# Kernel optimization log

Hardware: AMD Instinct MI355X
Metric: run time of the kernel (lower is better)

## Reference

```python
import jax, jax.numpy as jnp
import numpy as np

B, S, D = 4, 4096, 256


def setup_inputs() -> dict:
    key = jax.random.key(0)
    ks = jax.random.split(key, 7)
    s = 1.0 / np.sqrt(D)
    return {
        "x": jax.random.normal(ks[0], (B, S, D), dtype=jnp.float32),
        "Wq": jax.random.uniform(ks[1], (D, D), jnp.float32, -s, s),
        "bq": jax.random.uniform(ks[2], (D,), jnp.float32, -s, s),
        "Wk": jax.random.uniform(ks[3], (D, D), jnp.float32, -s, s),
        "bk": jax.random.uniform(ks[4], (D,), jnp.float32, -s, s),
        "Wv": jax.random.uniform(ks[5], (D, D), jnp.float32, -s, s),
        "bv": jax.random.uniform(ks[6], (D,), jnp.float32, -s, s),
    }


def reference(x, Wq, bq, Wk, bk, Wv, bv):
    # nn.Linear: y = x @ W.T + b
    Q = jnp.einsum("bsd,ed->bse", x, Wq) + bq
    K = jnp.einsum("bsd,ed->bse", x, Wk) + bk
    V = jnp.einsum("bsd,ed->bse", x, Wv) + bv
    dk = Q.shape[-1]
    scores = jnp.einsum("bqd,bkd->bqk", Q, K) / jnp.sqrt(jnp.float32(dk))
    # NOTE: original applies softmax over dim=1 (the query axis), not -1.
    attn = jax.nn.softmax(scores, axis=1)
    out = jnp.einsum("bqk,bkd->bqd", attn, V)
    return out
```

## Files before the change

### kernel.cpp

```cpp
#include <hip/hip_runtime.h>

typedef short bf16x8 __attribute__((ext_vector_type(8)));
typedef float f32x4 __attribute__((ext_vector_type(4)));
typedef unsigned short u16;

#define S_LEN 4096
#define D_DIM 256
#define NROW  16384

__device__ __forceinline__ u16 f2bf(float f) {
    union { float f; unsigned u; } v; v.f = f;
    unsigned r = v.u + 0x7FFFu + ((v.u >> 16) & 1u);
    return (u16)(r >> 16);
}

__device__ __forceinline__ size_t fr_qk(int t, int kk) {
    return (size_t)t * 4096 + kk * 512;
}
__device__ __forceinline__ size_t fr_v(int p, int dt, int kk2) {
    return (size_t)p * 16384 + (dt * 2 + kk2) * 512;
}

__device__ __forceinline__ void gll16(const u16* g, u16* l) {
    __builtin_amdgcn_global_load_lds(
        (const __attribute__((address_space(1))) unsigned int*)g,
        (__attribute__((address_space(3))) unsigned int*)l, 16, 0, 0);
}

#define WAITV4 asm volatile("s_waitcnt vmcnt(4)" ::: "memory")
#define WAITV0 asm volatile("s_waitcnt vmcnt(0)" ::: "memory")
#define WAITLGKM0 asm volatile("s_waitcnt lgkmcnt(0)" ::: "memory")
#define MEMFENCE asm volatile("" ::: "memory")

__global__ __launch_bounds__(256) void wconv(
    const float* __restrict__ Wq, const float* __restrict__ Wk,
    const float* __restrict__ Wv, u16* __restrict__ Wf)
{
    int i = blockIdx.x * 256 + threadIdx.x;
    int m = i >> 13;
    int idx = i & 8191;
    int ocol = idx >> 5;
    int d0 = (idx & 31) * 8;
    const float* s = (m == 0 ? Wq : (m == 1 ? Wk : Wv)) + ocol * 256 + d0;
    float4 v0 = *reinterpret_cast<const float4*>(s);
    float4 v1 = *reinterpret_cast<const float4*>(s + 4);
    union { ushort4 h[2]; int4 q; } t;
    t.h[0] = make_ushort4(f2bf(v0.x), f2bf(v0.y), f2bf(v0.z), f2bf(v0.w));
    t.h[1] = make_ushort4(f2bf(v1.x), f2bf(v1.y), f2bf(v1.z), f2bf(v1.w));
    size_t off = (size_t)m * 65536 + fr_qk(ocol >> 4, d0 >> 5)
               + ((d0 >> 3) & 3) * 128 + (ocol & 15) * 8;
    *reinterpret_cast<int4*>(Wf + off) = t.q;
}

__global__ __launch_bounds__(256) void qkv_proj(
    const float* __restrict__ x, const u16* __restrict__ Wf,
    const float* __restrict__ bq, const float* __restrict__ bk,
    const float* __restrict__ bv,
    u16* __restrict__ Qf, u16* __restrict__ Kf, u16* __restrict__ Vf)
{
    __shared__ u16 xs[32][264];
    const int tid = threadIdx.x;
    const int r0 = blockIdx.x * 32;

    #pragma unroll
    for (int i = 0; i < 8; ++i) {
        int c = i * 256 + tid;
        int row = c >> 6, c4 = c & 63;
        float4 v = reinterpret_cast<const float4*>(x + (size_t)(r0 + row) * D_DIM)[c4];
        *reinterpret_cast<ushort4*>(&xs[row][c4 * 4]) =
            make_ushort4(f2bf(v.x), f2bf(v.y), f2bf(v.z), f2bf(v.w));
    }
    __syncthreads();

    const int w = tid >> 6, l = tid & 63, lr = l & 15, lg = l >> 4;
    const int c0 = w * 64;

    bf16x8 a[2][8];
    #pragma unroll
    for (int qs = 0; qs < 2; ++qs)
        #pragma unroll
        for (int kk = 0; kk < 8; ++kk)
            a[qs][kk] = *reinterpret_cast<const bf16x8*>(&xs[qs * 16 + lr][kk * 32 + lg * 8]);

    const float* Bs[3] = {bq, bk, bv};

    #pragma unroll
    for (int m = 0; m < 3; ++m) {
        const u16* Wm = Wf + (size_t)m * 65536;
        f32x4 acc[2][4] = {};
        #pragma unroll
        for (int kk = 0; kk < 8; ++kk) {
            #pragma unroll
            for (int cf = 0; cf < 4; ++cf) {
                bf16x8 wfr = *reinterpret_cast<const bf16x8*>(
                    Wm + fr_qk(w * 4 + cf, kk) + l * 8);
                acc[0][cf] = __builtin_amdgcn_mfma_f32_16x16x32_bf16(a[0][kk], wfr, acc[0][cf], 0, 0, 0);
                acc[1][cf] = __builtin_amdgcn_mfma_f32_16x16x32_bf16(a[1][kk], wfr, acc[1][cf], 0, 0, 0);
            }
        }
        if (m < 2) {
            u16* outp = (m == 0) ? Qf : Kf;
            int t = r0 >> 4;
            #pragma unroll
            for (int qs = 0; qs < 2; ++qs) {
                #pragma unroll
                for (int cf = 0; cf < 4; ++cf) {
                    int col = c0 + cf * 16 + lr;
                    float bias = Bs[m][col];
                    size_t base = fr_qk(t + qs, col >> 5) + ((col >> 3) & 3) * 128 + (col & 7);
                    #pragma unroll
                    for (int r = 0; r < 4; ++r)
                        outp[base + (lg * 4 + r) * 8] = f2bf(acc[qs][cf][r] + bias);
                }
            }
        } else {
            int p  = (r0 >> 12) * 64 + ((r0 & 4095) >> 6);
            int kb = r0 & 63;
            #pragma unroll
            for (int qs = 0; qs < 2; ++qs) {
                #pragma unroll
                for (int cf = 0; cf < 4; ++cf) {
                    int d = c0 + cf * 16 + lr;
                    float bias = bv[d];
                    #pragma unroll
                    for (int r = 0; r < 4; ++r) {
                        int key = kb + qs * 16 + lg * 4 + r;
                        size_t off = fr_v(p, d >> 4, key >> 5)
                                   + ((key >> 3) & 3) * 128 + (d & 15) * 8 + (key & 7);
                        Vf[off] = f2bf(acc[qs][cf][r] + bias);
                    }
                }
            }
        }
    }
}

__global__ __launch_bounds__(256, 2) void col_denom(
    const u16* __restrict__ Qf, const u16* __restrict__ Kf, float* __restrict__ Zp)
{
    __shared__ __align__(16) u16 Qls[2][8192];
    const int tid = threadIdx.x, blk = blockIdx.x;
    const int xcd = blk & 7, sub = blk >> 3;
    const int b  = xcd >> 1;
    const int qq = ((xcd & 1) << 1) | (sub & 1);
    const int ktile = sub >> 1;
    const int w = tid >> 6, l = tid & 63, lr = l & 15, lg = l >> 4;
    const int k0 = ktile * 128;

    bf16x8 kreg[2][8];
    #pragma unroll
    for (int ks = 0; ks < 2; ++ks) {
        const int tk = b * 256 + (k0 >> 4) + w * 2 + ks;
        #pragma unroll
        for (int kk = 0; kk < 8; ++kk)
            kreg[ks][kk] = *reinterpret_cast<const bf16x8*>(Kf + fr_qk(tk, kk) + l * 8);
    }

    #define STAGE_Q(qt_, nb_) do { \
        const u16* g_ = Qf + ((size_t)(b * 256 + (qt_) * 2)) * 4096 + (w * 4) * 512 + l * 8; \
        u16* d_ = &Qls[nb_][(w * 4) * 512]; \
        _Pragma("unroll") \
        for (int f_ = 0; f_ < 4; ++f_) gll16(g_ + f_ * 512, d_ + f_ * 512); \
    } while (0)

    const int qt0 = qq * 32;
    STAGE_Q(qt0, 0);
    __syncthreads();

    float Z[2][4] = {};
    const float SC = 0.0625f;

    for (int it = 0; it < 32; ++it) {
        const int cur = it & 1;
        if (it < 31) STAGE_Q(qt0 + it + 1, cur ^ 1);

        f32x4 acc[2][2] = {};
        #pragma unroll
        for (int kk = 0; kk < 8; ++kk) {
            #pragma unroll
            for (int qf = 0; qf < 2; ++qf) {
                bf16x8 qfr = *reinterpret_cast<const bf16x8*>(
                    &Qls[cur][(qf * 8 + kk) * 512 + l * 8]);
                acc[0][qf] = __builtin_amdgcn_mfma_f32_16x16x32_bf16(kreg[0][kk], qfr, acc[0][qf], 0, 0, 0);
                acc[1][qf] = __builtin_amdgcn_mfma_f32_16x16x32_bf16(kreg[1][kk], qfr, acc[1][qf], 0, 0, 0);
            }
        }
        #pragma unroll
        for (int ks = 0; ks < 2; ++ks)
            #pragma unroll
            for (int qf = 0; qf < 2; ++qf)
                #pragma unroll
                for (int r = 0; r < 4; ++r)
                    Z[ks][r] += __expf(acc[ks][qf][r] * SC);
        __syncthreads();
    }

    #pragma unroll
    for (int ks = 0; ks < 2; ++ks) {
        #pragma unroll
        for (int r = 0; r < 4; ++r) {
            float z = Z[ks][r];
            z += __shfl_xor(z, 1);
            z += __shfl_xor(z, 2);
            z += __shfl_xor(z, 4);
            z += __shfl_xor(z, 8);
            if (lr == 0)
                Zp[qq * NROW + b * S_LEN + k0 + w * 32 + ks * 16 + lg * 4 + r] = z;
        }
    }
    #undef STAGE_Q
}

__global__ __launch_bounds__(256) void zlog(
    const float* __restrict__ Zp, float* __restrict__ LZ)
{
    int i = blockIdx.x * 256 + threadIdx.x;
    LZ[i] = logf(((Zp[i] + Zp[NROW + i]) + Zp[2 * NROW + i]) + Zp[3 * NROW + i]);
}

__global__ __launch_bounds__(512, 1) void attn_out(
    const u16* __restrict__ Qf, const u16* __restrict__ Kf, const u16* __restrict__ Vf,
    const float* __restrict__ LZ, float* __restrict__ out)
{
    __shared__ __align__(16) u16 Kls[3][8192];
    __shared__ __align__(16) u16 Vls[4][8192];
    __shared__ __align__(16) u16 ps[8][2][1280];
    __shared__ __align__(16) float lzs[1024];

    const int tid = threadIdx.x, blk = blockIdx.x;
    const int xcd = blk & 7, sub = blk >> 3;
    const int b  = xcd >> 1;
    const int kq = ((xcd & 1) << 1) | (sub & 1);
    const int qtile = sub >> 1;
    const int w = tid >> 6, l = tid & 63, lr = l & 15, lg = l >> 4;
    const int q0 = qtile * 256 + w * 32;
    const int base_tk = b * 256;
    const int kt0 = kq * 32;

    bf16x8 qreg[2][8];
    #pragma unroll
    for (int qs = 0; qs < 2; ++qs) {
        const int tq = base_tk + ((q0 + qs * 16) >> 4);
        #pragma unroll
        for (int kk = 0; kk < 8; ++kk)
            qreg[qs][kk] = *reinterpret_cast<const bf16x8*>(Qf + fr_qk(tq, kk) + l * 8);
    }

    #define STAGE(kt_) do { \
        if (w < 4) { \
            const u16* g_ = Kf + ((size_t)(base_tk + (kt0 + (kt_)) * 2)) * 4096 + (w * 4) * 512 + l * 8; \
            u16* d_ = &Kls[(kt_) % 3][(w * 4) * 512]; \
            _Pragma("unroll") \
            for (int f_ = 0; f_ < 4; ++f_) gll16(g_ + f_ * 512, d_ + f_ * 512); \
        } else { \
            const int kta_ = kt0 + (kt_); \
            const size_t vb_ = ((size_t)(b * 64 + (kta_ >> 1))) * 16384 + (kta_ & 1) * 512; \
            const int dt0_ = (w - 4) * 4; \
            _Pragma("unroll") \
            for (int f_ = 0; f_ < 4; ++f_) \
                gll16(Vf + vb_ + (size_t)(dt0_ + f_) * 1024 + l * 8, &Vls[(kt_) % 4][(dt0_ + f_) * 512]); \
        } \
    } while (0)

    #define QK(kt_) do { \
        const u16* kb_ = &Kls[(kt_) % 3][0]; \
        __builtin_amdgcn_s_setprio(1); \
        _Pragma("unroll") \
        for (int kk = 0; kk < 8; ++kk) { \
            bf16x8 k0_ = *reinterpret_cast<const bf16x8*>(kb_ + kk * 512 + l * 8); \
            bf16x8 k1_ = *reinterpret_cast<const bf16x8*>(kb_ + (8 + kk) * 512 + l * 8); \
            sacc[0][0] = __builtin_amdgcn_mfma_f32_16x16x32_bf16(qreg[0][kk], k0_, sacc[0][0], 0, 0, 0); \
            sacc[0][1] = __builtin_amdgcn_mfma_f32_16x16x32_bf16(qreg[1][kk], k0_, sacc[0][1], 0, 0, 0); \
            sacc[1][0] = __builtin_amdgcn_mfma_f32_16x16x32_bf16(qreg[0][kk], k1_, sacc[1][0], 0, 0, 0); \
            sacc[1][1] = __builtin_amdgcn_mfma_f32_16x16x32_bf16(qreg[1][kk], k1_, sacc[1][1], 0, 0, 0); \
        } \
        __builtin_amdgcn_s_setprio(0); \
    } while (0)

    #define PV(j_) do { \
        const u16* vb_ = &Vls[(j_) % 4][0]; \
        const u16* pb_ = &ps[w][(j_) & 1][0]; \
        bf16x8 af0_ = *reinterpret_cast<const bf16x8*>(pb_ + lr * 40 + lg * 8); \
        bf16x8 af1_ = *reinterpret_cast<const bf16x8*>(pb_ + (16 + lr) * 40 + lg * 8); \
        __builtin_amdgcn_s_setprio(1); \
        _Pragma("unroll") \
        for (int dt = 0; dt < 16; ++dt) { \
            bf16x8 vf_ = *reinterpret_cast<const bf16x8*>(vb_ + dt * 512 + l * 8); \
            oacc[0][dt] = __builtin_amdgcn_mfma_f32_16x16x32_bf16(af0_, vf_, oacc[0][dt], 0, 0, 0); \
            oacc[1][dt] = __builtin_amdgcn_mfma_f32_16x16x32_bf16(af1_, vf_, oacc[1][dt], 0, 0, 0); \
        } \
        __builtin_amdgcn_s_setprio(0); \
    } while (0)

    #define SM(kt_) do { \
        u16* pw_ = &ps[w][(kt_) & 1][0]; \
        _Pragma("unroll") \
        for (int cf = 0; cf < 2; ++cf) { \
            float Lv_ = lzs[(kt_) * 32 + cf * 16 + lr]; \
            _Pragma("unroll") \
            for (int qs = 0; qs < 2; ++qs) \
                _Pragma("unroll") \
                for (int r = 0; r < 4; ++r) { \
                    float p_ = __expf(fmaf(sacc[cf][qs][r], SC, -Lv_)); \
                    pw_[(qs * 16 + lg * 4 + r) * 40 + cf * 16 + lr] = f2bf(p_); \
                } \
        } \
    } while (0)

    f32x4 oacc[2][16] = {};
    const float SC = 0.0625f;

    f32x4 lzv;
    if (tid < 256)
        lzv = *reinterpret_cast<const f32x4*>(LZ + b * S_LEN + kt0 * 32 + tid * 4);
    STAGE(0);
    STAGE(1);
    if (tid < 256)
        *reinterpret_cast<f32x4*>(&lzs[tid * 4]) = lzv;
    WAITLGKM0;
    WAITV4;
    __builtin_amdgcn_s_barrier();
    MEMFENCE;

    #pragma unroll 1
    for (int kt = 0; kt < 30; ++kt) {
        STAGE(kt + 2);
        f32x4 sacc[2][2] = {};
        QK(kt);
        if (kt > 0) PV(kt - 1);
        SM(kt);
        WAITV4;
        __builtin_amdgcn_s_barrier();
        MEMFENCE;
    }
    {
        f32x4 sacc[2][2] = {};
        QK(30);
        PV(29);
        SM(30);
        WAITV0;
        __builtin_amdgcn_s_barrier();
        MEMFENCE;
    }
    {
        f32x4 sacc[2][2] = {};
        QK(31);
        PV(30);
        SM(31);
        PV(31);
    }

    #pragma unroll
    for (int qs = 0; qs < 2; ++qs) {
        #pragma unroll
        for (int dt = 0; dt < 16; ++dt) {
            #pragma unroll
            for (int r = 0; r < 4; ++r) {
                int row = q0 + qs * 16 + lg * 4 + r;
                unsafeAtomicAdd(&out[((size_t)(b * S_LEN + row)) * D_DIM + dt * 16 + lr],
                                oacc[qs][dt][r]);
            }
        }
    }
    #undef STAGE
    #undef QK
    #undef PV
    #undef SM
}

extern "C" void kernel_launch(void* const* d_in, const int* in_sizes, int n_in,
                              void* d_out, int out_size, void* d_ws, size_t ws_size,
                              hipStream_t stream) {
    const float* x  = (const float*)d_in[0];
    const float* Wq = (const float*)d_in[1];
    const float* bq = (const float*)d_in[2];
    const float* Wk = (const float*)d_in[3];
    const float* bk = (const float*)d_in[4];
    const float* Wv = (const float*)d_in[5];
    const float* bv = (const float*)d_in[6];
    float* out = (float*)d_out;

    u16* Qf = (u16*)d_ws;
    u16* Kf = Qf + (size_t)NROW * D_DIM;
    u16* Vf = Kf + (size_t)NROW * D_DIM;
    u16* Wf = Vf + (size_t)NROW * D_DIM;
    float* Zp = (float*)(Wf + 196608);
    float* LZ = Zp + 4 * NROW;

    hipMemsetAsync(out, 0, (size_t)NROW * D_DIM * sizeof(float), stream);

    wconv<<<96, 256, 0, stream>>>(Wq, Wk, Wv, Wf);
    qkv_proj<<<NROW / 32, 256, 0, stream>>>(x, Wf, bq, bk, bv, Qf, Kf, Vf);
    col_denom<<<512, 256, 0, stream>>>(Qf, Kf, Zp);
    zlog<<<NROW / 256, 256, 0, stream>>>(Zp, LZ);
    attn_out<<<256, 512, 0, stream>>>(Qf, Kf, Vf, LZ, out);
}
```

Baseline: 181.0 us.

## Materialize exp scores once, fold column normalizer into V, run plain PV GEMM

The score pass now writes the unnormalized exp(QK^T) matrix to workspace in bf16 MFMA fragment layout while it accumulates the column sums. Because the softmax runs over the query axis, the 1/Z factor belongs to each key, so it is folded into V by a small scaling kernel. A plain E·V' GEMM then replaces the second QK recompute and exp in attn_out. This removes the duplicated QK matmul and exponentials but adds a 128 MiB bf16 write and read of E, plus extra rounding of V. If the workspace is too small, the old recompute path runs instead.

```diff
diff --git a/kernel.cpp b/kernel.cpp
--- a/kernel.cpp
+++ b/kernel.cpp
@@ -13,12 +13,18 @@
     unsigned r = v.u + 0x7FFFu + ((v.u >> 16) & 1u);
     return (u16)(r >> 16);
 }
+__device__ __forceinline__ float bf2f(u16 h) {
+    union { unsigned u; float f; } v; v.u = ((unsigned)h) << 16; return v.f;
+}
 
 __device__ __forceinline__ size_t fr_qk(int t, int kk) {
     return (size_t)t * 4096 + kk * 512;
 }
 __device__ __forceinline__ size_t fr_v(int p, int dt, int kk2) {
     return (size_t)p * 16384 + (dt * 2 + kk2) * 512;
+}
+__device__ __forceinline__ size_t e_base(int b, int kc, int qt) {
+    return ((size_t)(b * 32768 + kc * 256 + qt)) * 512;
 }
 
 __device__ __forceinline__ void gll16(const u16* g, u16* l) {
@@ -27,6 +33,7 @@
         (__attribute__((address_space(3))) unsigned int*)l, 16, 0, 0);
 }
 
+#define WAITV6 asm volatile("s_waitcnt vmcnt(6)" ::: "memory")
 #define WAITV4 asm volatile("s_waitcnt vmcnt(4)" ::: "memory")
 #define WAITV0 asm volatile("s_waitcnt vmcnt(0)" ::: "memory")
 #define WAITLGKM0 asm volatile("s_waitcnt lgkmcnt(0)" ::: "memory")
@@ -135,8 +142,9 @@
     }
 }
 
-__global__ __launch_bounds__(256, 2) void col_denom(
-    const u16* __restrict__ Qf, const u16* __restrict__ Kf, float* __restrict__ Zp)
+__global__ __launch_bounds__(256, 2) void score_exp(
+    const u16* __restrict__ Qf, const u16* __restrict__ Kf,
+    u16* __restrict__ Ef, float* __restrict__ Zp, int write_e)
 {
     __shared__ __align__(16) u16 Qls[2][8192];
     const int tid = threadIdx.x, blk = blockIdx.x;
@@ -169,6 +177,7 @@
 
     float Z[2][4] = {};
     const float SC = 0.0625f;
+    const int kc = ktile * 4 + w;
 
     for (int it = 0; it < 32; ++it) {
         const int cur = it & 1;
@@ -186,12 +195,22 @@
             }
         }
         #pragma unroll
-        for (int ks = 0; ks < 2; ++ks)
-            #pragma unroll
-            for (int qf = 0; qf < 2; ++qf)
-                #pragma unroll
-                for (int r = 0; r < 4; ++r)
-                    Z[ks][r] += __expf(acc[ks][qf][r] * SC);
+        for (int ks = 0; ks < 2; ++ks) {
+            #pragma unroll
+            for (int qf = 0; qf < 2; ++qf) {
+                float e0 = __expf(acc[ks][qf][0] * SC);
+                float e1 = __expf(acc[ks][qf][1] * SC);
+                float e2 = __expf(acc[ks][qf][2] * SC);
+                float e3 = __expf(acc[ks][qf][3] * SC);
+                Z[ks][0] += e0; Z[ks][1] += e1; Z[ks][2] += e2; Z[ks][3] += e3;
+                if (write_e) {
+                    size_t ad = e_base(b, kc, (qt0 + it) * 2 + qf)
+                              + (ks * 2 + (lg >> 1)) * 128 + lr * 8 + (lg & 1) * 4;
+                    *reinterpret_cast<ushort4*>(Ef + ad) =
+                        make_ushort4(f2bf(e0), f2bf(e1), f2bf(e2), f2bf(e3));
+                }
+            }
+        }
         __syncthreads();
     }
 
@@ -211,6 +230,13 @@
     #undef STAGE_Q
 }
 
+__global__ __launch_bounds__(256) void zrecip(
+    const float* __restrict__ Zp, float* __restrict__ rZ)
+{
+    int i = blockIdx.x * 256 + threadIdx.x;
+    rZ[i] = 1.0f / (((Zp[i] + Zp[NROW + i]) + Zp[2 * NROW + i]) + Zp[3 * NROW + i]);
+}
+
 __global__ __launch_bounds__(256) void zlog(
     const float* __restrict__ Zp, float* __restrict__ LZ)
 {
@@ -218,7 +244,98 @@
     LZ[i] = logf(((Zp[i] + Zp[NROW + i]) + Zp[2 * NROW + i]) + Zp[3 * NROW + i]);
 }
 
-__global__ __launch_bounds__(512, 1) void attn_out(
+__global__ __launch_bounds__(256) void vscale(
+    u16* __restrict__ Vf, const float* __restrict__ rZ)
+{
+    int i = blockIdx.x * 256 + threadIdx.x;
+    int frag = i >> 6, l8 = i & 63;
+    int p = frag >> 5, sub = frag & 31, kk2 = sub & 1;
+    int b = p >> 6, kt = p & 63;
+    int kbase = b * S_LEN + kt * 64 + kk2 * 32 + (l8 >> 4) * 8;
+    float4 rz0 = *reinterpret_cast<const float4*>(&rZ[kbase]);
+    float4 rz1 = *reinterpret_cast<const float4*>(&rZ[kbase + 4]);
+    ushort4* vp = reinterpret_cast<ushort4*>(Vf + (size_t)i * 8);
+    ushort4 a = vp[0], c = vp[1];
+    vp[0] = make_ushort4(f2bf(bf2f(a.x) * rz0.x), f2bf(bf2f(a.y) * rz0.y),
+                         f2bf(bf2f(a.z) * rz0.z), f2bf(bf2f(a.w) * rz0.w));
+    vp[1] = make_ushort4(f2bf(bf2f(c.x) * rz1.x), f2bf(bf2f(c.y) * rz1.y),
+                         f2bf(bf2f(c.z) * rz1.z), f2bf(bf2f(c.w) * rz1.w));
+}
+
+__global__ __launch_bounds__(256, 2) void pv_gemm(
+    const u16* __restrict__ Ef, const u16* __restrict__ Vf, float* __restrict__ out)
+{
+    __shared__ __align__(16) u16 Els[3][4096];
+    __shared__ __align__(16) u16 Vls[3][8192];
+
+    const int tid = threadIdx.x, blk = blockIdx.x;
+    const int xcd = blk & 7, qtile = blk >> 3;
+    const int b = xcd >> 1, kh = xcd & 1;
+    const int w = tid >> 6, l = tid & 63, lr = l & 15, lg = l >> 4;
+
+    #define STAGE(it_) do { \
+        if ((it_) < 64) { \
+            const int kc_ = kh * 64 + (it_); \
+            const int nb_ = (it_) % 3; \
+            const size_t vb_ = ((size_t)(b * 64 + (kc_ >> 1))) * 16384 + (kc_ & 1) * 512; \
+            _Pragma("unroll") \
+            for (int i_ = 0; i_ < 6; ++i_) { \
+                int f_ = w * 6 + i_; \
+                if (f_ < 8) { \
+                    gll16(Ef + e_base(b, kc_, qtile * 8 + f_) + l * 8, &Els[nb_][f_ * 512]); \
+                } else { \
+                    int dt_ = f_ - 8; \
+                    gll16(Vf + vb_ + (size_t)dt_ * 1024 + l * 8, &Vls[nb_][dt_ * 512]); \
+                } \
+            } \
+        } \
+    } while (0)
+
+    STAGE(0);
+    STAGE(1);
+    WAITV6;
+    __builtin_amdgcn_s_barrier();
+    MEMFENCE;
+
+    f32x4 acc[2][16] = {};
+
+    #pragma unroll 1
+    for (int it = 0; it < 64; ++it) {
+        STAGE(it + 2);
+        const int cur = it % 3;
+        bf16x8 ef0 = *reinterpret_cast<const bf16x8*>(&Els[cur][(w * 2) * 512 + l * 8]);
+        bf16x8 ef1 = *reinterpret_cast<const bf16x8*>(&Els[cur][(w * 2 + 1) * 512 + l * 8]);
+        __builtin_amdgcn_s_setprio(1);
+        #pragma unroll
+        for (int dt = 0; dt < 16; ++dt) {
+            bf16x8 vfr = *reinterpret_cast<const bf16x8*>(&Vls[cur][dt * 512 + l * 8]);
+            acc[0][dt] = __builtin_amdgcn_mfma_f32_16x16x32_bf16(ef0, vfr, acc[0][dt], 0, 0, 0);
+            acc[1][dt] = __builtin_amdgcn_mfma_f32_16x16x32_bf16(ef1, vfr, acc[1][dt], 0, 0, 0);
+        }
+        __builtin_amdgcn_s_setprio(0);
+        if (it < 62) { WAITV6; } else { WAITV0; }
+        if (it < 63) {
+            __builtin_amdgcn_s_barrier();
+            MEMFENCE;
+        }
+    }
+
+    const int qg = b * S_LEN + qtile * 128 + w * 32;
+    #pragma unroll
+    for (int qs = 0; qs < 2; ++qs) {
+        #pragma unroll
+        for (int dt = 0; dt < 16; ++dt) {
+            #pragma unroll
+            for (int r = 0; r < 4; ++r) {
+                unsafeAtomicAdd(&out[(size_t)(qg + qs * 16 + lg * 4 + r) * D_DIM + dt * 16 + lr],
+                                acc[qs][dt][r]);
+            }
+        }
+    }
+    #undef STAGE
+}
+
+__global__ __launch_bounds__(512, 1) void attn_out_fb(
     const u16* __restrict__ Qf, const u16* __restrict__ Kf, const u16* __restrict__ Vf,
     const float* __restrict__ LZ, float* __restrict__ out)
 {
@@ -335,19 +452,14 @@
     }
     {
         f32x4 sacc[2][2] = {};
-        QK(30);
-        PV(29);
-        SM(30);
+        QK(30); PV(29); SM(30);
         WAITV0;
         __builtin_amdgcn_s_barrier();
         MEMFENCE;
     }
     {
         f32x4 sacc[2][2] = {};
-        QK(31);
-        PV(30);
-        SM(31);
-        PV(31);
+        QK(31); PV(30); SM(31); PV(31);
     }
 
     #pragma unroll
@@ -385,13 +497,23 @@
     u16* Vf = Kf + (size_t)NROW * D_DIM;
     u16* Wf = Vf + (size_t)NROW * D_DIM;
     float* Zp = (float*)(Wf + 196608);
-    float* LZ = Zp + 4 * NROW;
+    float* rZ = Zp + 4 * NROW;
+    u16* Ef = (u16*)(rZ + NROW);
+
+    const size_t need = (size_t)((char*)Ef - (char*)d_ws) + (size_t)4 * 32768 * 512 * 2;
 
     hipMemsetAsync(out, 0, (size_t)NROW * D_DIM * sizeof(float), stream);
-
     wconv<<<96, 256, 0, stream>>>(Wq, Wk, Wv, Wf);
     qkv_proj<<<NROW / 32, 256, 0, stream>>>(x, Wf, bq, bk, bv, Qf, Kf, Vf);
-    col_denom<<<512, 256, 0, stream>>>(Qf, Kf, Zp);
-    zlog<<<NROW / 256, 256, 0, stream>>>(Zp, LZ);
-    attn_out<<<256, 512, 0, stream>>>(Qf, Kf, Vf, LZ, out);
-}
+
+    if (ws_size >= need) {
+        score_exp<<<512, 256, 0, stream>>>(Qf, Kf, Ef, Zp, 1);
+        zrecip<<<NROW / 256, 256, 0, stream>>>(Zp, rZ);
+        vscale<<<2048, 256, 0, stream>>>(Vf, rZ);
+        pv_gemm<<<256, 256, 0, stream>>>(Ef, Vf, out);
+    } else {
+        score_exp<<<512, 256, 0, stream>>>(Qf, Kf, Qf , Zp, 0);
+        zlog<<<NROW / 256, 256, 0, stream>>>(Zp, rZ);
+        attn_out_fb<<<256, 512, 0, stream>>>(Qf, Kf, Vf, rZ, out);
+    }
+}
```

Measured after the change: 175.8 us, median of 2. 1.03x faster.
